# Optimization experiments

Measured on AMD Instinct MI355X. Metric: run time of the kernel, lower is better.

The kernel has to match this reference:

```python
import jax, jax.numpy as jnp
import numpy as np

B, S, D = 4, 1024, 2048
H, KVH = 32, 8
HD = D // H            # 64
KVD = HD * KVH         # 512
RANK, ALPHA = 16, 32
LORA_SCALE = ALPHA / RANK


def setup_inputs() -> dict:
    key = jax.random.key(0)
    ks = jax.random.split(key, 14)
    x = jax.random.normal(ks[0], (B, S, D), dtype=jnp.float32)
    # RoPE tables (llama-style complex freqs as cos/sin)
    inv = 1.0 / (10000.0 ** (np.arange(0, HD, 2, dtype=np.float32) / HD))
    t = np.arange(S, dtype=np.float32)
    ang = np.outer(t, inv)  # [S, HD//2]
    freqs_cos = jnp.asarray(np.cos(ang))
    freqs_sin = jnp.asarray(np.sin(ang))
    s = 0.02
    Wq = jax.random.normal(ks[1], (D, D), dtype=jnp.float32) * s
    Wk = jax.random.normal(ks[2], (D, KVD), dtype=jnp.float32) * s
    Wv = jax.random.normal(ks[3], (D, KVD), dtype=jnp.float32) * s
    Wo = jax.random.normal(ks[4], (D, D), dtype=jnp.float32) * s
    qA = jax.random.normal(ks[5], (D, RANK), dtype=jnp.float32) * s
    qB = jax.random.normal(ks[6], (RANK, D), dtype=jnp.float32) * s
    kA = jax.random.normal(ks[7], (D, RANK), dtype=jnp.float32) * s
    kB = jax.random.normal(ks[8], (RANK, KVD), dtype=jnp.float32) * s
    vA = jax.random.normal(ks[9], (D, RANK), dtype=jnp.float32) * s
    vB = jax.random.normal(ks[10], (RANK, KVD), dtype=jnp.float32) * s
    return {"x": x, "freqs_cos": freqs_cos, "freqs_sin": freqs_sin,
            "Wq": Wq, "Wk": Wk, "Wv": Wv, "Wo": Wo,
            "qA": qA, "qB": qB, "kA": kA, "kB": kB, "vA": vA, "vB": vB}


def _rope(t, cos, sin):
    # t: [b, s, h, hd]; cos/sin: [s, hd//2]
    b, s, h, hd = t.shape
    t2 = t.reshape(b, s, h, hd // 2, 2)
    x0, x1 = t2[..., 0], t2[..., 1]
    c = cos[None, :, None, :]
    sn = sin[None, :, None, :]
    r0 = x0 * c - x1 * sn
    r1 = x0 * sn + x1 * c
    return jnp.stack([r0, r1], axis=-1).reshape(b, s, h, hd)


def reference(x, freqs_cos, freqs_sin, Wq, Wk, Wv, Wo, qA, qB, kA, kB, vA, vB):
    b, s, _ = x.shape
    # QKV projections + LoRA deltas
    q = x @ Wq + (x @ qA) @ qB * LORA_SCALE   # [b,s,D]
    k = x @ Wk + (x @ kA) @ kB * LORA_SCALE   # [b,s,KVD]
    v = x @ Wv + (x @ vA) @ vB * LORA_SCALE   # [b,s,KVD]
    q = q.reshape(b, s, H, HD)
    k = k.reshape(b, s, KVH, HD)
    v = v.reshape(b, s, KVH, HD)
    q = _rope(q, freqs_cos, freqs_sin)
    k = _rope(k, freqs_cos, freqs_sin)
    # GQA attention without materializing repeated K/V:
    rep = H // KVH
    qg = q.reshape(b, s, KVH, rep, HD)
    scale = 1.0 / jnp.sqrt(jnp.asarray(HD, dtype=x.dtype))
    scores = jnp.einsum('bsgrd,btgd->bgrst', qg, k) * scale  # [b,kvh,rep,s,s]
    causal = jnp.tril(jnp.ones((s, s), dtype=bool))
    scores = jnp.where(causal[None, None, None], scores, jnp.finfo(scores.dtype).min)
    attn = jax.nn.softmax(scores, axis=-1)
    ctx = jnp.einsum('bgrst,btgd->bsgrd', attn, v).reshape(b, s, D)
    return ctx @ Wo
```

## Files before the change

kernel.cpp:

```cpp
#include <hip/hip_runtime.h>

typedef unsigned short u16;
typedef unsigned int u32;
typedef __attribute__((ext_vector_type(8))) short short8;
typedef __attribute__((ext_vector_type(4))) float f32x4;
typedef __attribute__((ext_vector_type(4))) u16 u16x4;

#define LOG2E 1.4426950408889634f
#define SCL2 (0.125f * LOG2E)

static __device__ __forceinline__ float bf2f(u16 u) {
    return __uint_as_float(((unsigned)u) << 16);
}
static __device__ __forceinline__ u16 f2bf(float f) {
    unsigned u = __float_as_uint(f);
    unsigned r = (u + 0x7FFF + ((u >> 16) & 1)) >> 16;
    return (u16)r;
}
static __device__ __forceinline__ u32 cvtpk(float lo, float hi) {
    u32 r;
    asm("v_cvt_pk_bf16_f32 %0, %1, %2" : "=v"(r) : "v"(lo), "v"(hi));
    return r;
}
static __device__ __forceinline__ f32x4 mfma16(short8 a, short8 b, f32x4 c) {
    return __builtin_amdgcn_mfma_f32_16x16x32_bf16(a, b, c, 0, 0, 0);
}
static __device__ __forceinline__ void gload_lds16(const void* g, void* l) {
    __builtin_amdgcn_global_load_lds(
        (const __attribute__((address_space(1))) void*)g,
        (__attribute__((address_space(3))) void*)l, 16, 0, 0);
}

__global__ void cast_x_kernel(const float* __restrict__ x, u16* __restrict__ xb, int n) {
    int i = (blockIdx.x * blockDim.x + threadIdx.x) * 4;
    int stride = gridDim.x * blockDim.x * 4;
    for (; i < n; i += stride) {
        f32x4 v = *(const f32x4*)&x[i];
        u16x4 o;
        o.x = f2bf(v.x); o.y = f2bf(v.y); o.z = f2bf(v.z); o.w = f2bf(v.w);
        *(u16x4*)&xb[i] = o;
    }
}

__global__ void transpose_cast_kernel(const float* __restrict__ src, u16* __restrict__ dst,
                                      int R, int C) {
    __shared__ float tile[32][33];
    int c0 = blockIdx.x * 32, r0 = blockIdx.y * 32;
    int tx = threadIdx.x, ty = threadIdx.y;
    tile[ty][tx] = src[(size_t)(r0 + ty) * C + c0 + tx];
    __syncthreads();
    dst[(size_t)(c0 + ty) * R + r0 + tx] = f2bf(tile[tx][ty]);
}

__global__ void transpose_bf16_kernel(const u16* __restrict__ src, u16* __restrict__ dst,
                                      int R, int C) {
    __shared__ u16 tile[32][33];
    int c0 = blockIdx.x * 32, r0 = blockIdx.y * 32;
    int tx = threadIdx.x, ty = threadIdx.y;
    tile[ty][tx] = src[(size_t)(r0 + ty) * C + c0 + tx];
    __syncthreads();
    dst[(size_t)(c0 + ty) * R + r0 + tx] = tile[tx][ty];
}

__global__ void fused_wT_kernel(const float* __restrict__ W, const float* __restrict__ A,
                                const float* __restrict__ Bm, u16* __restrict__ dst,
                                int R, int C) {
    __shared__ float tile[32][33];
    __shared__ float As[32][17];
    __shared__ float Bs[16][33];
    int c0 = blockIdx.x * 32, r0 = blockIdx.y * 32;
    int tx = threadIdx.x, ty = threadIdx.y;
    tile[ty][tx] = W[(size_t)(r0 + ty) * C + c0 + tx];
    if (tx < 16) As[ty][tx] = A[(r0 + ty) * 16 + tx];
    if (ty < 16) Bs[ty][tx] = Bm[(size_t)ty * C + c0 + tx];
    __syncthreads();
    float acc = 0.0f;
#pragma unroll
    for (int rr = 0; rr < 16; ++rr) acc += As[tx][rr] * Bs[rr][ty];
    dst[(size_t)(c0 + ty) * R + r0 + tx] = f2bf(tile[tx][ty] + 2.0f * acc);
}

template <int MODE, int CN>
__global__ __launch_bounds__(256) void gemm_kernel(
    const u16* __restrict__ A, const u16* __restrict__ Bt, void* __restrict__ C0,
    void* __restrict__ C1, void* __restrict__ C2, int Nn,
    const float* __restrict__ cosb, const float* __restrict__ sinb) {
    constexpr int K = 2048;
    constexpr int NT = K / 64;
    __shared__ u16 As[2][128 * 64];
    __shared__ u16 Bs[2][128 * 64];
    const int tid = threadIdx.x;
    const int wid = tid >> 6, lane = tid & 63;
    const int flat = blockIdx.y * gridDim.x + blockIdx.x;
    const int xcd = flat & 7, local = flat >> 3;
    const int mbase = (((xcd & 3) << 3) + (local & 7)) * 128;
    const int nbase = ((xcd >> 2) * CN + (local >> 3)) * 128;
    const int wrow = (wid >> 1) * 64, wcol = (wid & 1) * 64;
    const int fr = lane & 15, hi = lane >> 4;
    const int l8 = lane >> 3;
    const int swc = ((lane & 7) ^ l8) * 8;
    const int rs = fr & 7;
    f32x4 acc[4][4] = {};
    const u16* Ag = A + (size_t)mbase * K;
    const u16* Bg = Bt + (size_t)nbase * K;

    auto STAGE = [&](int kt, int buf) {
#pragma unroll
        for (int i = 0; i < 4; ++i) {
            const int r8 = (i * 4 + wid) * 8;
            gload_lds16(&Ag[(size_t)(r8 + l8) * K + kt * 64 + swc], &As[buf][r8 * 64]);
            gload_lds16(&Bg[(size_t)(r8 + l8) * K + kt * 64 + swc], &Bs[buf][r8 * 64]);
        }
    };

    STAGE(0, 0);
    for (int kt = 0; kt < NT; ++kt) {
        const int cur = kt & 1;
        if (kt < NT - 1) {
            STAGE(kt + 1, cur ^ 1);
            asm volatile("s_waitcnt vmcnt(8)" ::: "memory");
        } else {
            asm volatile("s_waitcnt vmcnt(0)" ::: "memory");
        }
        __builtin_amdgcn_s_barrier();
#pragma unroll
        for (int ks = 0; ks < 2; ++ks) {
            short8 af[4], bfr[4];
#pragma unroll
            for (int i = 0; i < 4; ++i) {
                const int arow = wrow + i * 16 + fr;
                const int brow = wcol + i * 16 + fr;
                af[i]  = *(const short8*)&As[cur][arow * 64 + (((ks * 4 + hi) ^ rs) * 8)];
                bfr[i] = *(const short8*)&Bs[cur][brow * 64 + (((ks * 4 + hi) ^ rs) * 8)];
            }
#pragma unroll
            for (int mi = 0; mi < 4; ++mi)
#pragma unroll
                for (int ni = 0; ni < 4; ++ni)
                    acc[mi][ni] = mfma16(af[mi], bfr[ni], acc[mi][ni]);
        }
        __builtin_amdgcn_s_barrier();
    }
    const int rb = mbase + wrow + (hi << 2);
    const int cb = nbase + wcol + fr;
    if (MODE == 1) {
        float* C = (float*)C0;
#pragma unroll
        for (int mi = 0; mi < 4; ++mi)
#pragma unroll
            for (int j = 0; j < 4; ++j) {
                const size_t ro = (size_t)(rb + mi * 16 + j) * Nn;
#pragma unroll
                for (int ni = 0; ni < 4; ++ni) C[ro + cb + ni * 16] = acc[mi][ni][j];
            }
    } else {
        u16* C;
        int cs, cc, rope;
        if (nbase < 2048)      { C = (u16*)C0; cs = 2048; cc = cb;        rope = 1; }
        else if (nbase < 2560) { C = (u16*)C1; cs = 512;  cc = cb - 2048; rope = 2; }
        else                   { C = (u16*)C2; cs = 512;  cc = cb - 2560; rope = 0; }
        if (rope) {
            const float scale = (rope == 1) ? SCL2 : 1.0f;
            const bool odd = (lane & 1);
#pragma unroll
            for (int mi = 0; mi < 4; ++mi)
#pragma unroll
                for (int j = 0; j < 4; ++j) {
                    const int row = rb + mi * 16 + j;
                    const int s = row & 1023;
                    const float* cr = cosb + s * 32;
                    const float* sr = sinb + s * 32;
                    const size_t ro = (size_t)row * cs;
#pragma unroll
                    for (int ni = 0; ni < 4; ++ni) {
                        const int col = cc + ni * 16;
                        const int i0 = (col & 63) >> 1;
                        float v = acc[mi][ni][j];
                        float p = __shfl_xor(v, 1);
                        float cv = cr[i0], sv = sr[i0];
                        float r = odd ? (p * sv + v * cv) : (v * cv - p * sv);
                        C[ro + col] = f2bf(r * scale);
                    }
                }
        } else {
#pragma unroll
            for (int mi = 0; mi < 4; ++mi)
#pragma unroll
                for (int j = 0; j < 4; ++j) {
                    const size_t ro = (size_t)(rb + mi * 16 + j) * cs;
#pragma unroll
                    for (int ni = 0; ni < 4; ++ni) C[ro + cc + ni * 16] = f2bf(acc[mi][ni][j]);
                }
        }
    }
}

template <bool DIAG>
static __device__ __forceinline__ void attn_tile_step(
    const u16* __restrict__ Ksb, const u16* __restrict__ Vsb,
    const short8* qf, f32x4* o, float& m, float& l,
    int sq, int kvb, int wid, int fr, int hi) {
    f32x4 s[4];
    const int sw = fr & 7;
#pragma unroll
    for (int mi = 0; mi < 4; ++mi) {
        if (!DIAG || mi <= wid) {
            const int row = (mi * 16 + fr) * 64;
            short8 kf0 = *(const short8*)&Ksb[row + ((hi ^ sw) * 8)];
            short8 kf1 = *(const short8*)&Ksb[row + (((4 + hi) ^ sw) * 8)];
            f32x4 z = {};
            z = mfma16(kf0, qf[0], z);
            z = mfma16(kf1, qf[1], z);
#pragma unroll
            for (int j = 0; j < 4; ++j) {
                float val = z[j];
                if (DIAG && mi == wid && (kvb + mi * 16 + hi * 4 + j > sq)) val = -3.0e38f;
                s[mi][j] = val;
            }
        } else {
            s[mi][0] = -3.0e38f; s[mi][1] = -3.0e38f;
            s[mi][2] = -3.0e38f; s[mi][3] = -3.0e38f;
        }
    }
    float pmax = fmaxf(fmaxf(fmaxf(s[0][0], s[0][1]), fmaxf(s[0][2], s[0][3])),
                       fmaxf(fmaxf(s[1][0], s[1][1]), fmaxf(s[1][2], s[1][3])));
    pmax = fmaxf(pmax, fmaxf(fmaxf(fmaxf(s[2][0], s[2][1]), fmaxf(s[2][2], s[2][3])),
                             fmaxf(fmaxf(s[3][0], s[3][1]), fmaxf(s[3][2], s[3][3]))));
    pmax = fmaxf(pmax, __shfl_xor(pmax, 16));
    pmax = fmaxf(pmax, __shfl_xor(pmax, 32));
    if (__any(pmax > m + 8.0f)) {
        const float mnew = fmaxf(m, pmax);
        const float fsc = exp2f(m - mnew);
        l *= fsc;
        m = mnew;
#pragma unroll
        for (int dn = 0; dn < 4; ++dn)
#pragma unroll
            for (int j = 0; j < 4; ++j) o[dn][j] *= fsc;
    }
    float rs = 0.0f;
    u32 pk[4][2];
#pragma unroll
    for (int mi = 0; mi < 4; ++mi) {
        float p0 = exp2f(s[mi][0] - m);
        float p1 = exp2f(s[mi][1] - m);
        float p2 = exp2f(s[mi][2] - m);
        float p3 = exp2f(s[mi][3] - m);
        rs += (p0 + p1) + (p2 + p3);
        pk[mi][0] = cvtpk(p0, p1);
        pk[mi][1] = cvtpk(p2, p3);
    }
    rs += __shfl_xor(rs, 16);
    rs += __shfl_xor(rs, 32);
    l += rs;
    const int ksmax = DIAG ? (wid >> 1) : 1;
#pragma unroll
    for (int ks = 0; ks < 2; ++ks) {
        if (ks > ksmax) continue;
        u32 w0 = pk[2 * ks][0], w2 = pk[2 * ks + 1][0];
        u32 w1 = pk[2 * ks][1], w3 = pk[2 * ks + 1][1];
        asm volatile("v_permlane32_swap_b32 %0, %1" : "+v"(w0), "+v"(w2));
        asm volatile("v_permlane16_swap_b32 %0, %1" : "+v"(w0), "+v"(w2));
        asm volatile("v_permlane32_swap_b32 %0, %1" : "+v"(w1), "+v"(w3));
        asm volatile("v_permlane16_swap_b32 %0, %1" : "+v"(w1), "+v"(w3));
        union { u32 w[4]; short8 s8; } pu;
        pu.w[0] = w0; pu.w[1] = w1; pu.w[2] = w2; pu.w[3] = w3;
        short8 pf = pu.s8;
#pragma unroll
        for (int dn = 0; dn < 4; ++dn) {
            const int row = (dn * 16 + fr) * 64;
            short8 vf = *(const short8*)&Vsb[row + (((ks * 4 + hi) ^ sw) * 8)];
            o[dn] = mfma16(vf, pf, o[dn]);
        }
    }
}

__global__ __launch_bounds__(256) void attn_kernel(
    const u16* __restrict__ q, const u16* __restrict__ k, const u16* __restrict__ vt,
    u16* __restrict__ ctx) {
    __shared__ u16 Ks[2][64 * 64];
    __shared__ u16 Vs[2][64 * 64];
    const int jp = blockIdx.x, h = blockIdx.y, b = blockIdx.z;
    const int qtA = jp, qtB = 15 - jp;
    const int g = h >> 2;
    const int tid = threadIdx.x, wid = tid >> 6, lane = tid & 63;
    const int fr = lane & 15, hi = lane >> 4, fk = hi * 8;
    const int sqA = qtA * 64 + wid * 16 + fr;
    const int sqB = qtB * 64 + wid * 16 + fr;
    short8 qfA[2], qfB[2];
    {
        const u16* qp = &q[((size_t)(b * 1024 + sqA)) * 2048 + h * 64];
        qfA[0] = *(const short8*)&qp[fk];
        qfA[1] = *(const short8*)&qp[32 + fk];
        const u16* qp2 = &q[((size_t)(b * 1024 + sqB)) * 2048 + h * 64];
        qfB[0] = *(const short8*)&qp2[fk];
        qfB[1] = *(const short8*)&qp2[32 + fk];
    }
    f32x4 oA[4] = {}, oB[4] = {};
    float mA = -3.0e38f, lA = 0.0f, mB = -3.0e38f, lB = 0.0f;
    const u16* kbase = k + ((size_t)b * 1024) * 512 + g * 64;
    const u16* vbase = vt + ((size_t)(g * 64)) * 4096 + b * 1024;
    const int l8 = lane >> 3;
    const int sw8 = ((lane & 7) ^ l8) * 8;

    auto stage = [&](int kt, int buf) {
        const u16* kg = kbase + (size_t)(kt * 64) * 512;
        const u16* vg = vbase + kt * 64;
#pragma unroll
        for (int i = 0; i < 2; ++i) {
            const int r8 = (i * 4 + wid) * 8;
            gload_lds16(&kg[(size_t)(r8 + l8) * 512 + sw8], &Ks[buf][r8 * 64]);
            gload_lds16(&vg[(size_t)(r8 + l8) * 4096 + sw8], &Vs[buf][r8 * 64]);
        }
    };

    stage(0, 0);
    for (int kt = 0; kt <= qtB; ++kt) {
        const int cur = kt & 1;
        __syncthreads();
        if (kt < qtB) stage(kt + 1, cur ^ 1);
        const int kvb = kt * 64;
        if (kt < qtA)
            attn_tile_step<false>(Ks[cur], Vs[cur], qfA, oA, mA, lA, sqA, kvb, wid, fr, hi);
        else if (kt == qtA)
            attn_tile_step<true>(Ks[cur], Vs[cur], qfA, oA, mA, lA, sqA, kvb, wid, fr, hi);
        if (kt < qtB)
            attn_tile_step<false>(Ks[cur], Vs[cur], qfB, oB, mB, lB, sqB, kvb, wid, fr, hi);
        else
            attn_tile_step<true>(Ks[cur], Vs[cur], qfB, oB, mB, lB, sqB, kvb, wid, fr, hi);
    }
    {
        const float linv = 1.0f / lA;
        const size_t obase = ((size_t)(b * 1024 + sqA)) * 2048 + h * 64;
#pragma unroll
        for (int dn = 0; dn < 4; ++dn) {
            u16x4 w;
#pragma unroll
            for (int j = 0; j < 4; ++j) w[j] = f2bf(oA[dn][j] * linv);
            *(u16x4*)&ctx[obase + dn * 16 + hi * 4] = w;
        }
    }
    {
        const float linv = 1.0f / lB;
        const size_t obase = ((size_t)(b * 1024 + sqB)) * 2048 + h * 64;
#pragma unroll
        for (int dn = 0; dn < 4; ++dn) {
            u16x4 w;
#pragma unroll
            for (int j = 0; j < 4; ++j) w[j] = f2bf(oB[dn][j] * linv);
            *(u16x4*)&ctx[obase + dn * 16 + hi * 4] = w;
        }
    }
}

extern "C" void kernel_launch(void* const* d_in, const int* in_sizes, int n_in,
                              void* d_out, int out_size, void* d_ws, size_t ws_size,
                              hipStream_t stream) {
    const float* x    = (const float*)d_in[0];
    const float* fcos = (const float*)d_in[1];
    const float* fsin = (const float*)d_in[2];
    const float* Wq   = (const float*)d_in[3];
    const float* Wk   = (const float*)d_in[4];
    const float* Wv   = (const float*)d_in[5];
    const float* Wo   = (const float*)d_in[6];
    const float* qA   = (const float*)d_in[7];
    const float* qB   = (const float*)d_in[8];
    const float* kA   = (const float*)d_in[9];
    const float* kB   = (const float*)d_in[10];
    const float* vA   = (const float*)d_in[11];
    const float* vB   = (const float*)d_in[12];
    float* out = (float*)d_out;

    char* ws = (char*)d_ws;
    size_t off = 0;
    auto alloc = [&](size_t bytes) { char* p = ws + off; off += (bytes + 255) & ~(size_t)255; return p; };
    u16* xb     = (u16*)alloc((size_t)4096 * 2048 * 2);
    u16* WqkvT  = (u16*)alloc((size_t)3072 * 2048 * 2);
    u16* WoT    = (u16*)alloc((size_t)2048 * 2048 * 2);
    u16* qbuf   = (u16*)alloc((size_t)4096 * 2048 * 2);
    u16* kbuf   = (u16*)alloc((size_t)4096 * 512 * 2);
    u16* vbuf   = (u16*)alloc((size_t)4096 * 512 * 2);
    u16* VT2    = (u16*)alloc((size_t)512 * 4096 * 2);
    u16* ctx    = (u16*)alloc((size_t)4096 * 2048 * 2);

    cast_x_kernel<<<2048, 256, 0, stream>>>(x, xb, 4096 * 2048);

    dim3 tb(32, 32);
    fused_wT_kernel<<<dim3(64, 64), tb, 0, stream>>>(Wq, qA, qB, WqkvT, 2048, 2048);
    fused_wT_kernel<<<dim3(16, 64), tb, 0, stream>>>(Wk, kA, kB, WqkvT + (size_t)2048 * 2048, 2048, 512);
    fused_wT_kernel<<<dim3(16, 64), tb, 0, stream>>>(Wv, vA, vB, WqkvT + (size_t)2560 * 2048, 2048, 512);
    transpose_cast_kernel<<<dim3(64, 64), tb, 0, stream>>>(Wo, WoT, 2048, 2048);

    gemm_kernel<2, 12><<<dim3(32, 24), 256, 0, stream>>>(xb, WqkvT, qbuf, kbuf, vbuf, 3072, fcos, fsin);
    transpose_bf16_kernel<<<dim3(16, 128), tb, 0, stream>>>(vbuf, VT2, 4096, 512);

    attn_kernel<<<dim3(8, 32, 4), 256, 0, stream>>>(qbuf, kbuf, VT2, ctx);

    gemm_kernel<1, 8><<<dim3(32, 16), 256, 0, stream>>>(ctx, WoT, out, nullptr, nullptr, 2048, nullptr, nullptr);
}
```

Before: 221.8 us.

## Process two query heads per attention block and pack RoPE tables as bf16

Each attention block now handles two adjacent query heads that share one KV group. Every staged K/V tile is therefore reused for twice the work, and the grid is halved. Separately, cos/sin are packed into one u32 bf16 table so the QKV GEMM epilogue issues a single load per element instead of two fp32 loads. The trade-offs are higher register pressure from the doubled accumulators, fewer blocks (512) to fill the GPU, and slightly lower RoPE precision.

New measurement: 221.1 us. No clear change (-0.3%).

```diff
diff --git a/kernel.cpp b/kernel.cpp
--- a/kernel.cpp
+++ b/kernel.cpp
@@ -40,6 +40,12 @@
         o.x = f2bf(v.x); o.y = f2bf(v.y); o.z = f2bf(v.z); o.w = f2bf(v.w);
         *(u16x4*)&xb[i] = o;
     }
+}
+
+__global__ void rope_pack_kernel(const float* __restrict__ cosb, const float* __restrict__ sinb,
+                                 u32* __restrict__ tbl, int n) {
+    int i = blockIdx.x * blockDim.x + threadIdx.x;
+    if (i < n) tbl[i] = (u32)f2bf(cosb[i]) | ((u32)f2bf(sinb[i]) << 16);
 }
 
 __global__ void transpose_cast_kernel(const float* __restrict__ src, u16* __restrict__ dst,
@@ -84,7 +90,7 @@
 __global__ __launch_bounds__(256) void gemm_kernel(
     const u16* __restrict__ A, const u16* __restrict__ Bt, void* __restrict__ C0,
     void* __restrict__ C1, void* __restrict__ C2, int Nn,
-    const float* __restrict__ cosb, const float* __restrict__ sinb) {
+    const u32* __restrict__ ropetbl) {
     constexpr int K = 2048;
     constexpr int NT = K / 64;
     __shared__ u16 As[2][128 * 64];
@@ -162,24 +168,22 @@
         if (rope) {
             const float scale = (rope == 1) ? SCL2 : 1.0f;
             const bool odd = (lane & 1);
+            const int ib = (fr >> 1);
 #pragma unroll
             for (int mi = 0; mi < 4; ++mi)
 #pragma unroll
                 for (int j = 0; j < 4; ++j) {
                     const int row = rb + mi * 16 + j;
-                    const int s = row & 1023;
-                    const float* cr = cosb + s * 32;
-                    const float* sr = sinb + s * 32;
+                    const u32* tr = ropetbl + (row & 1023) * 32;
                     const size_t ro = (size_t)row * cs;
 #pragma unroll
                     for (int ni = 0; ni < 4; ++ni) {
-                        const int col = cc + ni * 16;
-                        const int i0 = (col & 63) >> 1;
+                        u32 cspk = tr[ib + 8 * ni];
+                        float cv = bf2f((u16)cspk), sv = bf2f((u16)(cspk >> 16));
                         float v = acc[mi][ni][j];
                         float p = __shfl_xor(v, 1);
-                        float cv = cr[i0], sv = sr[i0];
                         float r = odd ? (p * sv + v * cv) : (v * cv - p * sv);
-                        C[ro + col] = f2bf(r * scale);
+                        C[ro + cc + ni * 16] = f2bf(r * scale);
                     }
                 }
         } else {
@@ -280,24 +284,26 @@
     u16* __restrict__ ctx) {
     __shared__ u16 Ks[2][64 * 64];
     __shared__ u16 Vs[2][64 * 64];
-    const int jp = blockIdx.x, h = blockIdx.y, b = blockIdx.z;
+    const int jp = blockIdx.x, hp = blockIdx.y, b = blockIdx.z;
     const int qtA = jp, qtB = 15 - jp;
-    const int g = h >> 2;
+    const int h0 = hp * 2;
+    const int g = hp >> 1;
     const int tid = threadIdx.x, wid = tid >> 6, lane = tid & 63;
     const int fr = lane & 15, hi = lane >> 4, fk = hi * 8;
     const int sqA = qtA * 64 + wid * 16 + fr;
     const int sqB = qtB * 64 + wid * 16 + fr;
-    short8 qfA[2], qfB[2];
+    short8 qA0[2], qB0[2], qA1[2], qB1[2];
     {
-        const u16* qp = &q[((size_t)(b * 1024 + sqA)) * 2048 + h * 64];
-        qfA[0] = *(const short8*)&qp[fk];
-        qfA[1] = *(const short8*)&qp[32 + fk];
-        const u16* qp2 = &q[((size_t)(b * 1024 + sqB)) * 2048 + h * 64];
-        qfB[0] = *(const short8*)&qp2[fk];
-        qfB[1] = *(const short8*)&qp2[32 + fk];
-    }
-    f32x4 oA[4] = {}, oB[4] = {};
-    float mA = -3.0e38f, lA = 0.0f, mB = -3.0e38f, lB = 0.0f;
+        const u16* pa = &q[((size_t)(b * 1024 + sqA)) * 2048 + h0 * 64];
+        qA0[0] = *(const short8*)&pa[fk];      qA0[1] = *(const short8*)&pa[32 + fk];
+        qA1[0] = *(const short8*)&pa[64 + fk]; qA1[1] = *(const short8*)&pa[96 + fk];
+        const u16* pb = &q[((size_t)(b * 1024 + sqB)) * 2048 + h0 * 64];
+        qB0[0] = *(const short8*)&pb[fk];      qB0[1] = *(const short8*)&pb[32 + fk];
+        qB1[0] = *(const short8*)&pb[64 + fk]; qB1[1] = *(const short8*)&pb[96 + fk];
+    }
+    f32x4 oA0[4] = {}, oA1[4] = {}, oB0[4] = {}, oB1[4] = {};
+    float mA0 = -3.0e38f, lA0 = 0.0f, mA1 = -3.0e38f, lA1 = 0.0f;
+    float mB0 = -3.0e38f, lB0 = 0.0f, mB1 = -3.0e38f, lB1 = 0.0f;
     const u16* kbase = k + ((size_t)b * 1024) * 512 + g * 64;
     const u16* vbase = vt + ((size_t)(g * 64)) * 4096 + b * 1024;
     const int l8 = lane >> 3;
@@ -320,37 +326,36 @@
         __syncthreads();
         if (kt < qtB) stage(kt + 1, cur ^ 1);
         const int kvb = kt * 64;
-        if (kt < qtA)
-            attn_tile_step<false>(Ks[cur], Vs[cur], qfA, oA, mA, lA, sqA, kvb, wid, fr, hi);
-        else if (kt == qtA)
-            attn_tile_step<true>(Ks[cur], Vs[cur], qfA, oA, mA, lA, sqA, kvb, wid, fr, hi);
-        if (kt < qtB)
-            attn_tile_step<false>(Ks[cur], Vs[cur], qfB, oB, mB, lB, sqB, kvb, wid, fr, hi);
-        else
-            attn_tile_step<true>(Ks[cur], Vs[cur], qfB, oB, mB, lB, sqB, kvb, wid, fr, hi);
-    }
-    {
-        const float linv = 1.0f / lA;
-        const size_t obase = ((size_t)(b * 1024 + sqA)) * 2048 + h * 64;
+        if (kt < qtA) {
+            attn_tile_step<false>(Ks[cur], Vs[cur], qA0, oA0, mA0, lA0, sqA, kvb, wid, fr, hi);
+            attn_tile_step<false>(Ks[cur], Vs[cur], qA1, oA1, mA1, lA1, sqA, kvb, wid, fr, hi);
+        } else if (kt == qtA) {
+            attn_tile_step<true>(Ks[cur], Vs[cur], qA0, oA0, mA0, lA0, sqA, kvb, wid, fr, hi);
+            attn_tile_step<true>(Ks[cur], Vs[cur], qA1, oA1, mA1, lA1, sqA, kvb, wid, fr, hi);
+        }
+        if (kt < qtB) {
+            attn_tile_step<false>(Ks[cur], Vs[cur], qB0, oB0, mB0, lB0, sqB, kvb, wid, fr, hi);
+            attn_tile_step<false>(Ks[cur], Vs[cur], qB1, oB1, mB1, lB1, sqB, kvb, wid, fr, hi);
+        } else {
+            attn_tile_step<true>(Ks[cur], Vs[cur], qB0, oB0, mB0, lB0, sqB, kvb, wid, fr, hi);
+            attn_tile_step<true>(Ks[cur], Vs[cur], qB1, oB1, mB1, lB1, sqB, kvb, wid, fr, hi);
+        }
+    }
+    auto emit = [&](const f32x4* o, float l, int sq, int h) {
+        const float linv = 1.0f / l;
+        const size_t obase = ((size_t)(b * 1024 + sq)) * 2048 + h * 64;
 #pragma unroll
         for (int dn = 0; dn < 4; ++dn) {
             u16x4 w;
 #pragma unroll
-            for (int j = 0; j < 4; ++j) w[j] = f2bf(oA[dn][j] * linv);
+            for (int j = 0; j < 4; ++j) w[j] = f2bf(o[dn][j] * linv);
             *(u16x4*)&ctx[obase + dn * 16 + hi * 4] = w;
         }
-    }
-    {
-        const float linv = 1.0f / lB;
-        const size_t obase = ((size_t)(b * 1024 + sqB)) * 2048 + h * 64;
-#pragma unroll
-        for (int dn = 0; dn < 4; ++dn) {
-            u16x4 w;
-#pragma unroll
-            for (int j = 0; j < 4; ++j) w[j] = f2bf(oB[dn][j] * linv);
-            *(u16x4*)&ctx[obase + dn * 16 + hi * 4] = w;
-        }
-    }
+    };
+    emit(oA0, lA0, sqA, h0);
+    emit(oA1, lA1, sqA, h0 + 1);
+    emit(oB0, lB0, sqB, h0);
+    emit(oB1, lB1, sqB, h0 + 1);
 }
 
 extern "C" void kernel_launch(void* const* d_in, const int* in_sizes, int n_in,
@@ -382,8 +387,10 @@
     u16* vbuf   = (u16*)alloc((size_t)4096 * 512 * 2);
     u16* VT2    = (u16*)alloc((size_t)512 * 4096 * 2);
     u16* ctx    = (u16*)alloc((size_t)4096 * 2048 * 2);
+    u32* rtbl   = (u32*)alloc((size_t)1024 * 32 * 4);
 
     cast_x_kernel<<<2048, 256, 0, stream>>>(x, xb, 4096 * 2048);
+    rope_pack_kernel<<<128, 256, 0, stream>>>(fcos, fsin, rtbl, 1024 * 32);
 
     dim3 tb(32, 32);
     fused_wT_kernel<<<dim3(64, 64), tb, 0, stream>>>(Wq, qA, qB, WqkvT, 2048, 2048);
@@ -391,10 +398,10 @@
     fused_wT_kernel<<<dim3(16, 64), tb, 0, stream>>>(Wv, vA, vB, WqkvT + (size_t)2560 * 2048, 2048, 512);
     transpose_cast_kernel<<<dim3(64, 64), tb, 0, stream>>>(Wo, WoT, 2048, 2048);
 
-    gemm_kernel<2, 12><<<dim3(32, 24), 256, 0, stream>>>(xb, WqkvT, qbuf, kbuf, vbuf, 3072, fcos, fsin);
+    gemm_kernel<2, 12><<<dim3(32, 24), 256, 0, stream>>>(xb, WqkvT, qbuf, kbuf, vbuf, 3072, rtbl);
     transpose_bf16_kernel<<<dim3(16, 128), tb, 0, stream>>>(vbuf, VT2, 4096, 512);
 
-    attn_kernel<<<dim3(8, 32, 4), 256, 0, stream>>>(qbuf, kbuf, VT2, ctx);
-
-    gemm_kernel<1, 8><<<dim3(32, 16), 256, 0, stream>>>(ctx, WoT, out, nullptr, nullptr, 2048, nullptr, nullptr);
-}
+    attn_kernel<<<dim3(8, 16, 4), 256, 0, stream>>>(qbuf, kbuf, VT2, ctx);
+
+    gemm_kernel<1, 8><<<dim3(32, 16), 256, 0, stream>>>(ctx, WoT, out, nullptr, nullptr, 2048, nullptr);
+}
```
